# Kernel tuning notes

Hardware: AMD Instinct MI355X
Metric: run time of the kernel (lower is better)

## Reference

```python
import jax, jax.numpy as jnp
import numpy as np

B, M, T, N = 128, 256, 512, 512

def setup_inputs() -> dict:
    key = jax.random.key(0)
    ks = jax.random.split(key, 6)
    return {
        "hidden_state": jax.random.normal(ks[0], (B, M), jnp.float32),
        "cell_state": jax.random.normal(ks[1], (B, M), jnp.float32),
        "X": jax.random.normal(ks[2], (B, T, N), jnp.float32),
        "We1": jax.random.normal(ks[3], (2 * M, T), jnp.float32) * 0.05,
        "be1": jnp.zeros((T,), jnp.float32),
        "We2": jax.random.normal(ks[4], (T, T), jnp.float32) * 0.05,
        "be2": jnp.zeros((T,), jnp.float32),
        "v": jax.random.normal(ks[5], (T, 1), jnp.float32) * 0.05,
        "bv": jnp.zeros((1,), jnp.float32),
    }

def reference(hidden_state, cell_state, X, We1, be1, We2, be2, v, bv):
    # concat hidden + cell: [B, 2m]; Dense(T) then broadcast over n (K.repeat)
    hc = jnp.concatenate([hidden_state, cell_state], axis=-1)
    hs = (hc @ We1 + be1)[:, None, :]                 # [B, 1, T] (broadcast over n)
    # Permute X -> [B, n, T], Dense(T): contract over T
    ux = jnp.einsum('btn,tk->bnk', X, We2) + be2      # [B, n, T]
    # add + tanh + Dense(1) fused chain
    e = jnp.tanh(hs + ux) @ v + bv                    # [B, n, 1]
    # Permute -> [B, 1, n], softmax over last axis (n)
    attn = jax.nn.softmax(jnp.swapaxes(e, 1, 2), axis=-1)  # [B, 1, n]
    return attn
```

## Files before the change

### kernel.cpp

```cpp
#include <hip/hip_runtime.h>
#include <hip/hip_bf16.h>


typedef _Float16 half8 __attribute__((ext_vector_type(8)));
typedef float floatx4 __attribute__((ext_vector_type(4)));

__device__ __forceinline__ float fast_tanh(float x) {
    float cx = fminf(15.0f, fmaxf(-15.0f, x));
    float e = __expf(2.0f * cx);
    return (e - 1.0f) * __fdividef(1.0f, e + 1.0f);
}

__global__ __launch_bounds__(256) void k_prep_a(const float* __restrict__ We2,
                                                _Float16* __restrict__ Af) {
    __shared__ float tile[64][65];
    const int t0 = (blockIdx.x & 7) << 6;
    const int k0 = (blockIdx.x >> 3) << 6;
    const int c  = threadIdx.x & 63;
    const int rb = threadIdx.x >> 6;
#pragma unroll
    for (int i = 0; i < 16; ++i) {
        int r = (i << 2) + rb;
        tile[r][c] = We2[(t0 + r) * 512 + k0 + c];
    }
    __syncthreads();
#pragma unroll
    for (int i = 0; i < 2; ++i) {
        int id   = threadIdx.x + (i << 8);
        int kbl  = id >> 7;
        int tsl  = (id >> 6) & 1;
        int lane = id & 63;
        int kloc = kbl * 16 + (lane & 15);
        int tloc = tsl * 32 + (lane >> 4) * 8;
        half8 h;
#pragma unroll
        for (int j = 0; j < 8; ++j) h[j] = (_Float16)tile[tloc + j][kloc];
        int kb = (k0 >> 4) + kbl;
        int ts = (t0 >> 5) + tsl;
        *(half8*)&Af[(((size_t)kb * 16 + ts) * 64 + lane) * 8] = h;
    }
}

__global__ __launch_bounds__(256) void k_hs(const float* __restrict__ hidden,
                                            const float* __restrict__ cell,
                                            const float* __restrict__ We1,
                                            const float* __restrict__ be1,
                                            const float* __restrict__ be2,
                                            float* __restrict__ g) {
    __shared__ __align__(16) float hcl[8][512];
    __shared__ float red[4][8][64];
    const int b0 = (blockIdx.x >> 3) << 3;
    const int k0 = (blockIdx.x & 7) << 6;
    for (int idx = threadIdx.x; idx < 8 * 512; idx += 256) {
        int bi = idx >> 9, j = idx & 511;
        hcl[bi][j] = (j < 256) ? hidden[(b0 + bi) * 256 + j]
                               : cell[(b0 + bi) * 256 + j - 256];
    }
    __syncthreads();
    const int kl = threadIdx.x & 63;
    const int jc = threadIdx.x >> 6;
    const int k  = k0 + kl;
    float acc[8] = {};
    for (int j = jc * 128; j < jc * 128 + 128; j += 4) {
        float w0 = We1[(j + 0) * 512 + k];
        float w1 = We1[(j + 1) * 512 + k];
        float w2 = We1[(j + 2) * 512 + k];
        float w3 = We1[(j + 3) * 512 + k];
#pragma unroll
        for (int bi = 0; bi < 8; ++bi) {
            float4 h = *(const float4*)&hcl[bi][j];
            acc[bi] += h.x * w0 + h.y * w1 + h.z * w2 + h.w * w3;
        }
    }
#pragma unroll
    for (int bi = 0; bi < 8; ++bi) red[jc][bi][kl] = acc[bi];
    __syncthreads();
    for (int idx = threadIdx.x; idx < 512; idx += 256) {
        int bi = idx >> 6, kk = idx & 63;
        float s = red[0][bi][kk] + red[1][bi][kk] + red[2][bi][kk] + red[3][bi][kk];
        int kg = k0 + kk;
        g[(b0 + bi) * 512 + kg] = s + be1[kg] + be2[kg];
    }
}

__global__ __launch_bounds__(512, 4) void k_main(const float* __restrict__ X,
                                                 const _Float16* __restrict__ Af,
                                                 const float* __restrict__ g,
                                                 const float* __restrict__ vvec,
                                                 float* __restrict__ E) {
    __shared__ __align__(16) _Float16 XT[32 * 512];
    const int b    = blockIdx.x >> 4;
    const int n0   = (blockIdx.x & 15) << 5;
    const int tid  = threadIdx.x;
    const int lane = tid & 63;
    const int wv   = tid >> 6;

    {
        const float* Xb = X + (size_t)b * (512 * 512);
        const int nl = tid & 31;
        const int tg = tid >> 5;
#pragma unroll
        for (int p = 0; p < 4; ++p) {
            int t0 = p * 128 + tg * 8;
            float f[8];
#pragma unroll
            for (int i = 0; i < 8; ++i) f[i] = Xb[(size_t)(t0 + i) * 512 + n0 + nl];
            half8 h;
#pragma unroll
            for (int i = 0; i < 8; ++i) h[i] = (_Float16)f[i];
            *(half8*)&XT[nl * 512 + (t0 ^ ((nl & 7) << 3))] = h;
        }
    }
    __syncthreads();

    const int l16 = lane & 15;
    const int lhi = lane >> 4;
    floatx4 acc[4][2];
#pragma unroll
    for (int a = 0; a < 4; ++a)
#pragma unroll
        for (int c = 0; c < 2; ++c) acc[a][c] = (floatx4){0.f, 0.f, 0.f, 0.f};

    const _Float16* __restrict__ Ap = Af + (size_t)wv * 32768 + (size_t)lane * 8;

    half8 afA[4], afB[4], bfA[2], bfB[2];
#pragma unroll
    for (int kf = 0; kf < 4; ++kf) afA[kf] = *(const half8*)&Ap[(size_t)kf * 8192];
#pragma unroll
    for (int nf = 0; nf < 2; ++nf) {
        int n = nf * 16 + l16;
        bfA[nf] = *(const half8*)&XT[n * 512 + ((lhi * 8) ^ ((n & 7) << 3))];
    }

    for (int ts = 0; ts < 16; ts += 2) {
#pragma unroll
        for (int kf = 0; kf < 4; ++kf)
            afB[kf] = *(const half8*)&Ap[(size_t)kf * 8192 + (ts + 1) * 512];
#pragma unroll
        for (int nf = 0; nf < 2; ++nf) {
            int n  = nf * 16 + l16;
            int t0 = (ts + 1) * 32 + lhi * 8;
            bfB[nf] = *(const half8*)&XT[n * 512 + (t0 ^ ((n & 7) << 3))];
        }
#pragma unroll
        for (int kf = 0; kf < 4; ++kf)
#pragma unroll
            for (int nf = 0; nf < 2; ++nf)
                acc[kf][nf] = __builtin_amdgcn_mfma_f32_16x16x32_f16(afA[kf], bfA[nf], acc[kf][nf], 0, 0, 0);
        if (ts + 2 < 16) {
#pragma unroll
            for (int kf = 0; kf < 4; ++kf)
                afA[kf] = *(const half8*)&Ap[(size_t)kf * 8192 + (ts + 2) * 512];
#pragma unroll
            for (int nf = 0; nf < 2; ++nf) {
                int n  = nf * 16 + l16;
                int t0 = (ts + 2) * 32 + lhi * 8;
                bfA[nf] = *(const half8*)&XT[n * 512 + (t0 ^ ((n & 7) << 3))];
            }
        }
#pragma unroll
        for (int kf = 0; kf < 4; ++kf)
#pragma unroll
            for (int nf = 0; nf < 2; ++nf)
                acc[kf][nf] = __builtin_amdgcn_mfma_f32_16x16x32_f16(afB[kf], bfB[nf], acc[kf][nf], 0, 0, 0);
    }

    const float* gb = g + b * 512;
    float s0 = 0.f, s1 = 0.f;
#pragma unroll
    for (int kf = 0; kf < 4; ++kf) {
        const int kb = wv * 64 + kf * 16 + lhi * 4;
        float g0 = gb[kb + 0], g1 = gb[kb + 1], g2 = gb[kb + 2], g3 = gb[kb + 3];
        float v0 = vvec[kb + 0], v1 = vvec[kb + 1], v2 = vvec[kb + 2], v3 = vvec[kb + 3];
        s0 += fast_tanh(acc[kf][0][0] + g0) * v0;
        s0 += fast_tanh(acc[kf][0][1] + g1) * v1;
        s0 += fast_tanh(acc[kf][0][2] + g2) * v2;
        s0 += fast_tanh(acc[kf][0][3] + g3) * v3;
        s1 += fast_tanh(acc[kf][1][0] + g0) * v0;
        s1 += fast_tanh(acc[kf][1][1] + g1) * v1;
        s1 += fast_tanh(acc[kf][1][2] + g2) * v2;
        s1 += fast_tanh(acc[kf][1][3] + g3) * v3;
    }
    s0 += __shfl_xor(s0, 16);  s0 += __shfl_xor(s0, 32);
    s1 += __shfl_xor(s1, 16);  s1 += __shfl_xor(s1, 32);

    __syncthreads();
    float* ered = (float*)XT;
    if (lane < 16) {
        ered[wv * 32 + l16]      = s0;
        ered[wv * 32 + 16 + l16] = s1;
    }
    __syncthreads();
    if (tid < 32) {
        float e = 0.f;
#pragma unroll
        for (int w = 0; w < 8; ++w) e += ered[w * 32 + tid];
        E[b * 512 + n0 + tid] = e;
    }
}

__global__ __launch_bounds__(256) void k_softmax(const float* __restrict__ E,
                                                 float* __restrict__ out) {
    __shared__ float rmax[4], rsum[4];
    const int b = blockIdx.x;
    const int tid = threadIdx.x;
    float e0 = E[b * 512 + tid];
    float e1 = E[b * 512 + 256 + tid];
    float m = fmaxf(e0, e1);
    for (int o = 32; o > 0; o >>= 1) m = fmaxf(m, __shfl_xor(m, o));
    if ((tid & 63) == 0) rmax[tid >> 6] = m;
    __syncthreads();
    m = fmaxf(fmaxf(rmax[0], rmax[1]), fmaxf(rmax[2], rmax[3]));
    float p0 = __expf(e0 - m), p1 = __expf(e1 - m);
    float ss = p0 + p1;
    for (int o = 32; o > 0; o >>= 1) ss += __shfl_xor(ss, o);
    if ((tid & 63) == 0) rsum[tid >> 6] = ss;
    __syncthreads();
    ss = rsum[0] + rsum[1] + rsum[2] + rsum[3];
    float inv = __fdividef(1.0f, ss);
    out[b * 512 + tid] = p0 * inv;
    out[b * 512 + 256 + tid] = p1 * inv;
}

extern "C" void kernel_launch(void* const* d_in, const int* in_sizes, int n_in,
                              void* d_out, int out_size, void* d_ws, size_t ws_size,
                              hipStream_t stream) {
    const float* hidden = (const float*)d_in[0];
    const float* cell   = (const float*)d_in[1];
    const float* X      = (const float*)d_in[2];
    const float* We1    = (const float*)d_in[3];
    const float* be1    = (const float*)d_in[4];
    const float* We2    = (const float*)d_in[5];
    const float* be2    = (const float*)d_in[6];
    const float* v      = (const float*)d_in[7];
    float* out = (float*)d_out;

    char* ws = (char*)d_ws;
    _Float16* Af = (_Float16*)ws;
    float* g     = (float*)(ws + 524288);
    float* E     = (float*)(ws + 524288 + 262144);

    k_prep_a<<<64, 256, 0, stream>>>(We2, Af);
    k_hs<<<128, 256, 0, stream>>>(hidden, cell, We1, be1, be2, g);
    k_main<<<2048, 512, 0, stream>>>(X, Af, g, v, E);
    k_softmax<<<128, 256, 0, stream>>>(E, out);
}
```

Before: 88.26 us.

## Halve k_main block to 4 waves with 128 output columns each, relayout Af

k_main now runs 256 threads (4 waves) per block, and each wave computes 128 of the T outputs (8 A fragments) instead of 64. Each B fragment read from LDS therefore feeds twice as many MFMAs. The A-operand layout produced by k_prep_a is reorganised so that for each t-step a wave's fragments sit contiguously, and k_prep_a runs as 16 blocks each handling a 32-row slice. The X staging loop is reordered so each thread loads contiguous runs of t. The larger accumulator and fragment register sets raise register pressure and lower the occupancy hint from 4 to 3, and fewer waves per block may hide the X load latency less well.

```diff
diff --git a/kernel.cpp b/kernel.cpp
--- a/kernel.cpp
+++ b/kernel.cpp
@@ -13,31 +13,21 @@
 
 __global__ __launch_bounds__(256) void k_prep_a(const float* __restrict__ We2,
                                                 _Float16* __restrict__ Af) {
-    __shared__ float tile[64][65];
-    const int t0 = (blockIdx.x & 7) << 6;
-    const int k0 = (blockIdx.x >> 3) << 6;
-    const int c  = threadIdx.x & 63;
-    const int rb = threadIdx.x >> 6;
-#pragma unroll
-    for (int i = 0; i < 16; ++i) {
-        int r = (i << 2) + rb;
-        tile[r][c] = We2[(t0 + r) * 512 + k0 + c];
-    }
-    __syncthreads();
-#pragma unroll
-    for (int i = 0; i < 2; ++i) {
-        int id   = threadIdx.x + (i << 8);
-        int kbl  = id >> 7;
-        int tsl  = (id >> 6) & 1;
-        int lane = id & 63;
-        int kloc = kbl * 16 + (lane & 15);
-        int tloc = tsl * 32 + (lane >> 4) * 8;
+    __shared__ float w2[32][512];
+    const int ts = blockIdx.x;
+    for (int idx = threadIdx.x; idx < 32 * 512; idx += 256) {
+        int tl = idx >> 9, k = idx & 511;
+        w2[tl][k] = We2[(ts * 32 + tl) * 512 + k];
+    }
+    __syncthreads();
+    for (int item = threadIdx.x; item < 32 * 64; item += 256) {
+        int c = item >> 6, l = item & 63;
+        int k  = c * 16 + (l & 15);
+        int tl = (l >> 4) * 8;
         half8 h;
 #pragma unroll
-        for (int j = 0; j < 8; ++j) h[j] = (_Float16)tile[tloc + j][kloc];
-        int kb = (k0 >> 4) + kbl;
-        int ts = (t0 >> 5) + tsl;
-        *(half8*)&Af[(((size_t)kb * 16 + ts) * 64 + lane) * 8] = h;
+        for (int j = 0; j < 8; ++j) h[j] = (_Float16)w2[tl + j][k];
+        *(half8*)&Af[(((size_t)ts * 32 + c) * 64 + l) * 8] = h;
     }
 }
 
@@ -83,7 +73,7 @@
     }
 }
 
-__global__ __launch_bounds__(512, 4) void k_main(const float* __restrict__ X,
+__global__ __launch_bounds__(256, 3) void k_main(const float* __restrict__ X,
                                                  const _Float16* __restrict__ Af,
                                                  const float* __restrict__ g,
                                                  const float* __restrict__ vvec,
@@ -94,82 +84,87 @@
     const int tid  = threadIdx.x;
     const int lane = tid & 63;
     const int wv   = tid >> 6;
+    const int l16  = lane & 15;
+    const int lhi  = lane >> 4;
 
     {
-        const float* Xb = X + (size_t)b * (512 * 512);
+        const float* Xb = X + (size_t)b * (512 * 512) + n0;
         const int nl = tid & 31;
         const int tg = tid >> 5;
-#pragma unroll
-        for (int p = 0; p < 4; ++p) {
-            int t0 = p * 128 + tg * 8;
+#pragma unroll 2
+        for (int oct = 0; oct < 8; ++oct) {
+            int t0 = tg * 64 + oct * 8;
             float f[8];
 #pragma unroll
-            for (int i = 0; i < 8; ++i) f[i] = Xb[(size_t)(t0 + i) * 512 + n0 + nl];
+            for (int j = 0; j < 8; ++j) f[j] = Xb[(size_t)(t0 + j) * 512 + nl];
             half8 h;
 #pragma unroll
-            for (int i = 0; i < 8; ++i) h[i] = (_Float16)f[i];
+            for (int j = 0; j < 8; ++j) h[j] = (_Float16)f[j];
             *(half8*)&XT[nl * 512 + (t0 ^ ((nl & 7) << 3))] = h;
         }
     }
     __syncthreads();
 
-    const int l16 = lane & 15;
-    const int lhi = lane >> 4;
-    floatx4 acc[4][2];
-#pragma unroll
-    for (int a = 0; a < 4; ++a)
-#pragma unroll
-        for (int c = 0; c < 2; ++c) acc[a][c] = (floatx4){0.f, 0.f, 0.f, 0.f};
-
-    const _Float16* __restrict__ Ap = Af + (size_t)wv * 32768 + (size_t)lane * 8;
-
-    half8 afA[4], afB[4], bfA[2], bfB[2];
-#pragma unroll
-    for (int kf = 0; kf < 4; ++kf) afA[kf] = *(const half8*)&Ap[(size_t)kf * 8192];
-#pragma unroll
-    for (int nf = 0; nf < 2; ++nf) {
-        int n = nf * 16 + l16;
-        bfA[nf] = *(const half8*)&XT[n * 512 + ((lhi * 8) ^ ((n & 7) << 3))];
-    }
-
-    for (int ts = 0; ts < 16; ts += 2) {
-#pragma unroll
-        for (int kf = 0; kf < 4; ++kf)
-            afB[kf] = *(const half8*)&Ap[(size_t)kf * 8192 + (ts + 1) * 512];
-#pragma unroll
-        for (int nf = 0; nf < 2; ++nf) {
-            int n  = nf * 16 + l16;
-            int t0 = (ts + 1) * 32 + lhi * 8;
-            bfB[nf] = *(const half8*)&XT[n * 512 + (t0 ^ ((n & 7) << 3))];
-        }
-#pragma unroll
-        for (int kf = 0; kf < 4; ++kf)
-#pragma unroll
-            for (int nf = 0; nf < 2; ++nf)
-                acc[kf][nf] = __builtin_amdgcn_mfma_f32_16x16x32_f16(afA[kf], bfA[nf], acc[kf][nf], 0, 0, 0);
-        if (ts + 2 < 16) {
-#pragma unroll
-            for (int kf = 0; kf < 4; ++kf)
-                afA[kf] = *(const half8*)&Ap[(size_t)kf * 8192 + (ts + 2) * 512];
-#pragma unroll
-            for (int nf = 0; nf < 2; ++nf) {
-                int n  = nf * 16 + l16;
-                int t0 = (ts + 2) * 32 + lhi * 8;
-                bfA[nf] = *(const half8*)&XT[n * 512 + (t0 ^ ((n & 7) << 3))];
-            }
-        }
-#pragma unroll
-        for (int kf = 0; kf < 4; ++kf)
-#pragma unroll
-            for (int nf = 0; nf < 2; ++nf)
-                acc[kf][nf] = __builtin_amdgcn_mfma_f32_16x16x32_f16(afB[kf], bfB[nf], acc[kf][nf], 0, 0, 0);
+    floatx4 acc[8][2];
+#pragma unroll
+    for (int a = 0; a < 8; ++a) {
+        acc[a][0] = (floatx4){0.f, 0.f, 0.f, 0.f};
+        acc[a][1] = (floatx4){0.f, 0.f, 0.f, 0.f};
+    }
+
+    const _Float16* __restrict__ Ap = Af + (size_t)wv * 4096 + (size_t)lane * 8;
+    const int bsw0 = ((0 * 16 + l16) & 7) << 3;
+    const int bsw1 = ((1 * 16 + l16) & 7) << 3;
+    const int brow0 = (0 * 16 + l16) * 512;
+    const int brow1 = (1 * 16 + l16) * 512;
+
+    half8 aA[8], aB[8], bA[2], bB[2];
+#pragma unroll
+    for (int kf = 0; kf < 8; ++kf) aA[kf] = *(const half8*)&Ap[(size_t)kf * 512];
+    {
+        int t0 = lhi * 8;
+        bA[0] = *(const half8*)&XT[brow0 + (t0 ^ bsw0)];
+        bA[1] = *(const half8*)&XT[brow1 + (t0 ^ bsw1)];
+    }
+
+#pragma unroll
+    for (int tp = 0; tp < 8; ++tp) {
+        const int ts0 = tp * 2;
+        {
+            const size_t ao = (size_t)(ts0 + 1) * 16384;
+#pragma unroll
+            for (int kf = 0; kf < 8; ++kf)
+                aB[kf] = *(const half8*)&Ap[ao + (size_t)kf * 512];
+            int t0 = (ts0 + 1) * 32 + lhi * 8;
+            bB[0] = *(const half8*)&XT[brow0 + (t0 ^ bsw0)];
+            bB[1] = *(const half8*)&XT[brow1 + (t0 ^ bsw1)];
+        }
+#pragma unroll
+        for (int kf = 0; kf < 8; ++kf) {
+            acc[kf][0] = __builtin_amdgcn_mfma_f32_16x16x32_f16(aA[kf], bA[0], acc[kf][0], 0, 0, 0);
+            acc[kf][1] = __builtin_amdgcn_mfma_f32_16x16x32_f16(aA[kf], bA[1], acc[kf][1], 0, 0, 0);
+        }
+        if (tp < 7) {
+            const size_t ao = (size_t)(ts0 + 2) * 16384;
+#pragma unroll
+            for (int kf = 0; kf < 8; ++kf)
+                aA[kf] = *(const half8*)&Ap[ao + (size_t)kf * 512];
+            int t0 = (ts0 + 2) * 32 + lhi * 8;
+            bA[0] = *(const half8*)&XT[brow0 + (t0 ^ bsw0)];
+            bA[1] = *(const half8*)&XT[brow1 + (t0 ^ bsw1)];
+        }
+#pragma unroll
+        for (int kf = 0; kf < 8; ++kf) {
+            acc[kf][0] = __builtin_amdgcn_mfma_f32_16x16x32_f16(aB[kf], bB[0], acc[kf][0], 0, 0, 0);
+            acc[kf][1] = __builtin_amdgcn_mfma_f32_16x16x32_f16(aB[kf], bB[1], acc[kf][1], 0, 0, 0);
+        }
     }
 
     const float* gb = g + b * 512;
     float s0 = 0.f, s1 = 0.f;
 #pragma unroll
-    for (int kf = 0; kf < 4; ++kf) {
-        const int kb = wv * 64 + kf * 16 + lhi * 4;
+    for (int kf = 0; kf < 8; ++kf) {
+        const int kb = wv * 128 + kf * 16 + lhi * 4;
         float g0 = gb[kb + 0], g1 = gb[kb + 1], g2 = gb[kb + 2], g3 = gb[kb + 3];
         float v0 = vvec[kb + 0], v1 = vvec[kb + 1], v2 = vvec[kb + 2], v3 = vvec[kb + 3];
         s0 += fast_tanh(acc[kf][0][0] + g0) * v0;
@@ -192,9 +187,7 @@
     }
     __syncthreads();
     if (tid < 32) {
-        float e = 0.f;
-#pragma unroll
-        for (int w = 0; w < 8; ++w) e += ered[w * 32 + tid];
+        float e = ered[tid] + ered[32 + tid] + ered[64 + tid] + ered[96 + tid];
         E[b * 512 + n0 + tid] = e;
     }
 }
@@ -240,8 +233,8 @@
     float* g     = (float*)(ws + 524288);
     float* E     = (float*)(ws + 524288 + 262144);
 
-    k_prep_a<<<64, 256, 0, stream>>>(We2, Af);
+    k_prep_a<<<16, 256, 0, stream>>>(We2, Af);
     k_hs<<<128, 256, 0, stream>>>(hidden, cell, We1, be1, be2, g);
-    k_main<<<2048, 512, 0, stream>>>(X, Af, g, v, E);
+    k_main<<<2048, 256, 0, stream>>>(X, Af, g, v, E);
     k_softmax<<<128, 256, 0, stream>>>(E, out);
 }
```

New measurement: 122.5 us. +38.8%, slower.
